# Kernel optimization log

Measured on AMD Instinct MI355X. Metric: run time of the kernel, lower is better.

## Reference

```python
import jax, jax.numpy as jnp
import numpy as np

B, CI, CO, K, SD, H, W = 8, 128, 128, 3, 512, 256, 256


def setup_inputs() -> dict:
    key = jax.random.key(0)
    k0, k1, k2, k3 = jax.random.split(key, 4)
    x = jax.random.normal(k0, (B, CI, H, W), jnp.float32)
    style = jax.random.normal(k1, (B, SD), jnp.float32)
    # learned params
    w_base = jax.random.normal(k2, (1, CO, CI, K, K), jnp.float32)   # ModulatedConv2d.weight
    aff_w = jax.random.normal(k3, (CI, SD), jnp.float32)             # affine weight [out=CI, in=SD]
    aff_b = jnp.ones((CI,), jnp.float32)                             # bias_init=1
    return {"x": x, "style": style, "w_base": w_base, "aff_w": aff_w, "aff_b": aff_b}


def reference(x, style, w_base, aff_w, aff_b):
    b, ci, h, w_ = x.shape
    co, k = w_base.shape[1], w_base.shape[3]
    # affine: FullyConnectedLayer, linear activation, weight_gain = 1/sqrt(style_dim)
    aff_gain = 1.0 / np.sqrt(aff_w.shape[1])
    s = style @ (aff_w * aff_gain).T + aff_b                 # [B, CI]
    # modulate
    wgain = 1.0 / np.sqrt(ci * k * k)
    wt = w_base * wgain * s[:, None, :, None, None]          # [B, CO, CI, K, K]
    # demodulate
    d = jax.lax.rsqrt(jnp.sum(wt * wt, axis=(2, 3, 4)) + 1e-8)  # [B, CO]
    wt = wt * d[:, :, None, None, None]
    # grouped conv, groups = batch, padding = k//2 (up=down=1 path)
    wt = wt.reshape(b * co, ci, k, k)
    xg = x.reshape(1, b * ci, h, w_)
    pad = k // 2
    y = jax.lax.conv_general_dilated(
        xg, wt, window_strides=(1, 1), padding=[(pad, pad), (pad, pad)],
        dimension_numbers=("NCHW", "OIHW", "NCHW"), feature_group_count=b)
    return y.reshape(b, co, h, w_)
```

## Files before the change

### kernel.cpp

```cpp
#include <hip/hip_runtime.h>
#include <stdint.h>

#define BB 8
#define SD 512

typedef unsigned short u16;
typedef __attribute__((ext_vector_type(8))) __bf16 bf16x8;
typedef __attribute__((ext_vector_type(16))) float f32x16;

__device__ float g_s[BB * 128];
__device__ u16 g_wtb[BB * 9 * 2 * 8192];
__device__ u16 g_xb[(size_t)BB * 258 * 258 * 128 + 2048];

typedef const __attribute__((address_space(1))) uint32_t* gp1;
typedef __attribute__((address_space(3))) uint32_t* lp3;

__device__ __forceinline__ void glds16(const void* g, void* l) {
    __builtin_amdgcn_global_load_lds((gp1)g, (lp3)l, 16, 0, 0);
}

__device__ __forceinline__ u16 f2bf(float f) {
    uint32_t u = __float_as_uint(f);
    u += 0x7FFFu + ((u >> 16) & 1u);
    return (u16)(u >> 16);
}

__global__ void affine_kernel(const float* __restrict__ style,
                              const float* __restrict__ aff_w,
                              const float* __restrict__ aff_b) {
    int b = blockIdx.x;
    int ci = threadIdx.x;
    const float gain = 0.044194173824159216f;
    const float* st = style + b * SD;
    const float* aw = aff_w + ci * SD;
    float acc = 0.f;
    #pragma unroll 8
    for (int j = 0; j < SD; ++j) acc += st[j] * aw[j];
    g_s[b * 128 + ci] = acc * gain + aff_b[ci];
}

__global__ __launch_bounds__(256) void modulate_kernel(const float* __restrict__ w_base) {
    int blk = blockIdx.x;
    int b = blk >> 7, co = blk & 127;
    int tid = threadIdx.x;
    const float wgain = 0.029462782549439483f;
    const int n = 1152;
    const float* wb = w_base + co * n;
    const float* sp = g_s + b * 128;

    float v[5];
    float sq = 0.f;
    #pragma unroll
    for (int i = 0; i < 5; ++i) {
        int idx = tid + i * 256;
        float w = 0.f;
        if (idx < n) {
            int ci = idx / 9;
            w = wb[idx] * wgain * sp[ci];
        }
        v[i] = w;
        sq += w * w;
    }
    #pragma unroll
    for (int off = 32; off > 0; off >>= 1) sq += __shfl_down(sq, off, 64);
    __shared__ float red[4];
    int lane = tid & 63, wvi = tid >> 6;
    if (lane == 0) red[wvi] = sq;
    __syncthreads();
    float tot = red[0] + red[1] + red[2] + red[3];
    float d = rsqrtf(tot + 1e-8f);
    #pragma unroll
    for (int i = 0; i < 5; ++i) {
        int idx = tid + i * 256;
        if (idx < n) {
            int ci = idx / 9;
            int k9 = idx - ci * 9;
            u16 hv = f2bf(v[i] * d);
            int slot = (ci & 63) >> 3, e = ci & 7;
            size_t base = ((size_t)(b * 9 + k9) * 2 + (ci >> 6)) * 8192;
            g_wtb[base + slot * 1024 + co * 8 + e] = hv;
        }
    }
}

__global__ __launch_bounds__(256) void zero_border_kernel() {
    int b = blockIdx.x;
    uint4 z = make_uint4(0, 0, 0, 0);
    char* xbB = (char*)g_xb;
    for (int i = threadIdx.x; i < 16448; i += 256) {
        size_t pix; int k;
        if (i < 4128)       { pix = (size_t)(b * 258 + 0)   * 258 + (i >> 4);            k = i & 15; }
        else if (i < 8256)  { int j = i - 4128;  pix = (size_t)(b * 258 + 257) * 258 + (j >> 4);       k = j & 15; }
        else if (i < 12352) { int j = i - 8256;  pix = (size_t)(b * 258 + 1 + (j >> 4)) * 258 + 0;     k = j & 15; }
        else                { int j = i - 12352; pix = (size_t)(b * 258 + 1 + (j >> 4)) * 258 + 257;   k = j & 15; }
        *(uint4*)(xbB + pix * 256 + (size_t)k * 16) = z;
    }
}

__global__ __launch_bounds__(256) void transpose_kernel(const float* __restrict__ x) {
    __shared__ __align__(16) u16 t_lds[64 * 128];
    const int chunk = blockIdx.x;
    const int gy = blockIdx.y;
    const int b = blockIdx.z;
    const int px0 = chunk * 64;
    const int tid = threadIdx.x;
    const int pq = tid & 15;
    const int cig = tid >> 4;

    const float* base = x + (size_t)b * 128 * 65536 + (size_t)gy * 256 + px0 + pq * 4;
    char* ldsB = (char*)t_lds;

    float4 v[8];
    #pragma unroll
    for (int c = 0; c < 8; ++c)
        v[c] = *(const float4*)(base + (size_t)(cig * 8 + c) * 65536);

    #pragma unroll
    for (int j = 0; j < 4; ++j) {
        uint32_t dw[4];
        #pragma unroll
        for (int d = 0; d < 4; ++d) {
            const float* lo4 = (const float*)&v[2 * d];
            const float* hi4 = (const float*)&v[2 * d + 1];
            dw[d] = (uint32_t)f2bf(lo4[j]) | ((uint32_t)f2bf(hi4[j]) << 16);
        }
        int px = pq * 4 + j;
        int key = (px0 + px + 1) & 7;
        int slot = cig ^ key;
        *(uint4*)(ldsB + px * 256 + slot * 16) = *(uint4*)dw;
    }
    __syncthreads();

    char* outB = (char*)g_xb;
    #pragma unroll
    for (int it = 0; it < 4; ++it) {
        int flat = it * 256 + tid;
        int r = flat >> 4, k = flat & 15;
        int key = (px0 + r + 1) & 7;
        uint4 val = *(const uint4*)(ldsB + r * 256 + ((k ^ key) << 4));
        size_t pix = ((size_t)(b * 258 + gy + 1)) * 258 + (px0 + r + 1);
        *(uint4*)(outB + pix * 256 + k * 16) = val;
    }
}

__global__ __launch_bounds__(512, 4) void conv_kernel(float* __restrict__ y) {
    __shared__ __align__(16) u16 xs[2720 * 8];
    __shared__ __align__(16) u16 ab[2][8192];

    const int b = blockIdx.y;
    const int t = blockIdx.x;
    const int swzt = (t & 7) * 32 + (t >> 3);
    const int tx = swzt & 7, ty = swzt >> 3;
    const int y0 = ty * 8, x0 = tx * 32;
    const int tid = threadIdx.x;
    const int lane = tid & 63, wv = tid >> 6;
    const int l31 = lane & 31;
    const int l5 = lane >> 5;
    const int coHalf = (wv & 1) * 64;
    const int py0w = (wv >> 1) * 2;

    const char* xbB = (const char*)g_xb;
    const char* wtbB = (const char*)(g_wtb) + (size_t)b * 294912;
    char* xsB = (char*)xs;

    f32x16 acc[2][2];
    #pragma unroll
    for (int mf = 0; mf < 2; ++mf)
        #pragma unroll
        for (int rf = 0; rf < 2; ++rf)
            acc[mf][rf] = (f32x16){0.f};

    uint4 va[6], vb[6];
    #pragma unroll
    for (int it = 0; it < 6; ++it) {
        int f = it * 512 + tid;
        if (f < 2720) {
            int p = f >> 3, s2 = f & 7;
            int row = p / 34, col = p - row * 34;
            size_t pix = (size_t)(b * 258 + y0 + row) * 258 + (x0 + col);
            va[it] = *(const uint4*)(xbB + pix * 256 + s2 * 16);
        }
    }
    #pragma unroll
    for (int it = 0; it < 6; ++it) {
        int f = it * 512 + tid;
        if (f < 2720) {
            int p = f >> 3, s2 = f & 7;
            *(uint4*)(xsB + (size_t)(s2 * 340 + p) * 16) = va[it];
        }
    }
    #pragma unroll
    for (int it = 0; it < 6; ++it) {
        int f = it * 512 + tid;
        if (f < 2720) {
            int p = f >> 3, s2 = f & 7;
            int row = p / 34, col = p - row * 34;
            size_t pix = (size_t)(b * 258 + y0 + row) * 258 + (x0 + col);
            vb[it] = *(const uint4*)(xbB + pix * 256 + 128 + s2 * 16);
        }
    }
    #pragma unroll
    for (int q = 0; q < 2; ++q) {
        int j = wv * 2 + q;
        glds16(wtbB + j * 1024 + lane * 16, (char*)ab[0] + j * 1024);
    }
    __syncthreads();

    #pragma unroll 1
    for (int s = 0; s < 18; ++s) {
        if (s < 17) {
            int ns = s + 1;
            int ntap = (ns >= 9) ? (ns - 9) : ns;
            int nh = (ns >= 9) ? 1 : 0;
            const char* src = wtbB + (ntap * 2 + nh) * 16384;
            char* dst = (char*)ab[ns & 1];
            #pragma unroll
            for (int q = 0; q < 2; ++q) {
                int j = wv * 2 + q;
                glds16(src + j * 1024 + lane * 16, dst + j * 1024);
            }
        }

        const int tap = (s >= 9) ? (s - 9) : s;
        const int ky = tap / 3, kx = tap - ky * 3;
        const char* abuf = (const char*)ab[s & 1];
        const int prow = (py0w + ky) * 34 + l31 + kx;

        #pragma unroll
        for (int ks = 0; ks < 4; ++ks) {
            const int cig = ks * 2 + l5;
            bf16x8 af[2];
            #pragma unroll
            for (int mf = 0; mf < 2; ++mf) {
                int co = coHalf + mf * 32 + l31;
                af[mf] = *(const bf16x8*)(abuf + cig * 2048 + co * 16);
            }
            bf16x8 bf[2];
            #pragma unroll
            for (int rf = 0; rf < 2; ++rf)
                bf[rf] = *(const bf16x8*)(xsB + (size_t)(cig * 340 + prow + rf * 34) * 16);
            __builtin_amdgcn_s_setprio(1);
            #pragma unroll
            for (int mf = 0; mf < 2; ++mf)
                #pragma unroll
                for (int rf = 0; rf < 2; ++rf)
                    acc[mf][rf] = __builtin_amdgcn_mfma_f32_32x32x16_bf16(
                        af[mf], bf[rf], acc[mf][rf], 0, 0, 0);
            __builtin_amdgcn_s_setprio(0);
        }
        __syncthreads();

        if (s == 8) {
            #pragma unroll
            for (int it = 0; it < 6; ++it) {
                int f = it * 512 + tid;
                if (f < 2720) {
                    int p = f >> 3, s2 = f & 7;
                    *(uint4*)(xsB + (size_t)(s2 * 340 + p) * 16) = vb[it];
                }
            }
            __syncthreads();
        }
    }

    float* yb = y + (size_t)b * 128 * 65536;
    #pragma unroll
    for (int mf = 0; mf < 2; ++mf) {
        #pragma unroll
        for (int rf = 0; rf < 2; ++rf) {
            int gy = y0 + py0w + rf;
            int gx = x0 + l31;
            #pragma unroll
            for (int j = 0; j < 16; ++j) {
                int co = coHalf + mf * 32 + (j & 3) + 8 * (j >> 2) + 4 * l5;
                yb[(size_t)co * 65536 + gy * 256 + gx] = acc[mf][rf][j];
            }
        }
    }
}

extern "C" void kernel_launch(void* const* d_in, const int* in_sizes, int n_in,
                              void* d_out, int out_size, void* d_ws, size_t ws_size,
                              hipStream_t stream) {
    const float* x = (const float*)d_in[0];
    const float* style = (const float*)d_in[1];
    const float* w_base = (const float*)d_in[2];
    const float* aff_w = (const float*)d_in[3];
    const float* aff_b = (const float*)d_in[4];
    float* y = (float*)d_out;

    affine_kernel<<<BB, 128, 0, stream>>>(style, aff_w, aff_b);
    modulate_kernel<<<BB * 128, 256, 0, stream>>>(w_base);
    zero_border_kernel<<<BB, 256, 0, stream>>>();
    transpose_kernel<<<dim3(4, 256, BB), 256, 0, stream>>>(x);
    conv_kernel<<<dim3(256, BB), 512, 0, stream>>>(y);
}
```

Measured before the change: 338.2 us.

## Deepen weight prefetch to a 4-stage ring with explicit vmcnt waits

Replaces the double-buffered per-tap weight staging with a ring of four half-size buffers, split into 36 sub-steps, and prefetches three stages ahead using global_load_lds. Synchronisation now uses manual s_waitcnt vmcnt/lgkmcnt plus raw s_barrier instead of __syncthreads, so the compiler no longer forces full drains of outstanding loads. The goal is to hide weight-load latency behind MFMA work. In exchange there are twice as many barriers, each covering half the MFMA work, and the hand-counted vmcnt values must stay correct, which is fragile given the other outstanding global loads such as the vb prefetch.

```diff
diff --git a/kernel.cpp b/kernel.cpp
--- a/kernel.cpp
+++ b/kernel.cpp
@@ -145,7 +145,7 @@
 
 __global__ __launch_bounds__(512, 4) void conv_kernel(float* __restrict__ y) {
     __shared__ __align__(16) u16 xs[2720 * 8];
-    __shared__ __align__(16) u16 ab[2][8192];
+    __shared__ __align__(16) u16 abr[4][4096];
 
     const int b = blockIdx.y;
     const int t = blockIdx.x;
@@ -199,58 +199,20 @@
             vb[it] = *(const uint4*)(xbB + pix * 256 + 128 + s2 * 16);
         }
     }
-    #pragma unroll
-    for (int q = 0; q < 2; ++q) {
-        int j = wv * 2 + q;
-        glds16(wtbB + j * 1024 + lane * 16, (char*)ab[0] + j * 1024);
-    }
-    __syncthreads();
-
-    #pragma unroll 1
-    for (int s = 0; s < 18; ++s) {
-        if (s < 17) {
-            int ns = s + 1;
-            int ntap = (ns >= 9) ? (ns - 9) : ns;
-            int nh = (ns >= 9) ? 1 : 0;
-            const char* src = wtbB + (ntap * 2 + nh) * 16384;
-            char* dst = (char*)ab[ns & 1];
-            #pragma unroll
-            for (int q = 0; q < 2; ++q) {
-                int j = wv * 2 + q;
-                glds16(src + j * 1024 + lane * 16, dst + j * 1024);
-            }
-        }
-
-        const int tap = (s >= 9) ? (s - 9) : s;
-        const int ky = tap / 3, kx = tap - ky * 3;
-        const char* abuf = (const char*)ab[s & 1];
-        const int prow = (py0w + ky) * 34 + l31 + kx;
-
-        #pragma unroll
-        for (int ks = 0; ks < 4; ++ks) {
-            const int cig = ks * 2 + l5;
-            bf16x8 af[2];
-            #pragma unroll
-            for (int mf = 0; mf < 2; ++mf) {
-                int co = coHalf + mf * 32 + l31;
-                af[mf] = *(const bf16x8*)(abuf + cig * 2048 + co * 16);
-            }
-            bf16x8 bf[2];
-            #pragma unroll
-            for (int rf = 0; rf < 2; ++rf)
-                bf[rf] = *(const bf16x8*)(xsB + (size_t)(cig * 340 + prow + rf * 34) * 16);
-            __builtin_amdgcn_s_setprio(1);
-            #pragma unroll
-            for (int mf = 0; mf < 2; ++mf)
-                #pragma unroll
-                for (int rf = 0; rf < 2; ++rf)
-                    acc[mf][rf] = __builtin_amdgcn_mfma_f32_32x32x16_bf16(
-                        af[mf], bf[rf], acc[mf][rf], 0, 0, 0);
-            __builtin_amdgcn_s_setprio(0);
-        }
-        __syncthreads();
-
-        if (s == 8) {
+    __builtin_amdgcn_sched_barrier(0);
+    #pragma unroll
+    for (int a = 0; a < 4; ++a) {
+        const char* src = wtbB + (size_t)(((a >> 1) * 4 + (a & 1)) * 8192);
+        glds16(src + tid * 16, (char*)abr[a] + tid * 16);
+    }
+    __builtin_amdgcn_sched_barrier(0);
+    asm volatile("s_waitcnt vmcnt(3) lgkmcnt(0)" ::: "memory");
+    __builtin_amdgcn_sched_barrier(0);
+    __builtin_amdgcn_s_barrier();
+
+    #pragma unroll
+    for (int s = 0; s < 36; ++s) {
+        if (s == 18) {
             #pragma unroll
             for (int it = 0; it < 6; ++it) {
                 int f = it * 512 + tid;
@@ -259,8 +221,58 @@
                     *(uint4*)(xsB + (size_t)(s2 * 340 + p) * 16) = vb[it];
                 }
             }
-            __syncthreads();
-        }
+            asm volatile("s_waitcnt lgkmcnt(0)" ::: "memory");
+            __builtin_amdgcn_sched_barrier(0);
+            __builtin_amdgcn_s_barrier();
+        }
+
+        const int u = s >> 1;
+        const int tap = (u >= 9) ? (u - 9) : u;
+        const int ky = tap / 3, kx = tap - ky * 3;
+        const int halfsel = s & 1;
+        const char* abuf = (const char*)abr[s & 3];
+        const int prow = (py0w + ky) * 34 + l31 + kx;
+
+        #pragma unroll
+        for (int ks = 0; ks < 2; ++ks) {
+            const int cl = ks * 2 + l5;
+            const int cig = halfsel * 4 + cl;
+            bf16x8 af[2];
+            #pragma unroll
+            for (int mf = 0; mf < 2; ++mf)
+                af[mf] = *(const bf16x8*)(abuf + (size_t)(cl * 128 + coHalf + mf * 32 + l31) * 16);
+            bf16x8 bfv[2];
+            #pragma unroll
+            for (int rf = 0; rf < 2; ++rf)
+                bfv[rf] = *(const bf16x8*)(xsB + (size_t)(cig * 340 + prow + rf * 34) * 16);
+            __builtin_amdgcn_s_setprio(1);
+            #pragma unroll
+            for (int mf = 0; mf < 2; ++mf)
+                #pragma unroll
+                for (int rf = 0; rf < 2; ++rf)
+                    acc[mf][rf] = __builtin_amdgcn_mfma_f32_32x32x16_bf16(
+                        af[mf], bfv[rf], acc[mf][rf], 0, 0, 0);
+            __builtin_amdgcn_s_setprio(0);
+        }
+
+        asm volatile("s_waitcnt lgkmcnt(0)" ::: "memory");
+        __builtin_amdgcn_sched_barrier(0);
+        __builtin_amdgcn_s_barrier();
+
+        if (s + 4 <= 35) {
+            const int w = s + 4, uw = w >> 1;
+            const int tw = (uw >= 9) ? (uw - 9) : uw;
+            const int hw = (uw >= 9) ? 1 : 0;
+            const char* src = wtbB + ((tw * 2 + hw) * 2 + (w & 1)) * 8192;
+            glds16(src + tid * 16, (char*)abr[s & 3] + tid * 16);
+        }
+        __builtin_amdgcn_sched_barrier(0);
+        if (s <= 31)      asm volatile("s_waitcnt vmcnt(3)" ::: "memory");
+        else if (s == 32) asm volatile("s_waitcnt vmcnt(2)" ::: "memory");
+        else if (s == 33) asm volatile("s_waitcnt vmcnt(1)" ::: "memory");
+        else if (s == 34) asm volatile("s_waitcnt vmcnt(0)" ::: "memory");
+        __builtin_amdgcn_sched_barrier(0);
+        __builtin_amdgcn_s_barrier();
     }
 
     float* yb = y + (size_t)b * 128 * 65536;
```

Result: slower. 420.8 us (+24.4%).
